# Optimization experiments

Measured on AMD Instinct MI355X. Metric: run time of the kernel, lower is better.

## Reference

```python
import jax, jax.numpy as jnp
import numpy as np
from jax import lax

B, P, NB, NF, NC, R = 128, 2048, 2000, 250, 16, 128
LS = NB - NF  # number of simulated bins = len_bins_gensig - 1


def setup_inputs() -> dict:
    key = jax.random.key(0)
    ks = jax.random.split(key, 10)
    return {
        'batched_stim_spat': jax.random.normal(ks[0], (B, P), jnp.float32),
        'stim_time': jax.random.normal(ks[1], (NB,), jnp.float32),
        'batched_initial_spike_section': (jax.random.uniform(ks[2], (B, NF)) < 0.05).astype(jnp.float32),
        'batched_coupling_cells': (jax.random.uniform(ks[3], (B, NC, NB)) < 0.05).astype(jnp.float32),
        'spatial_filter': jax.random.normal(ks[4], (P,), jnp.float32) * 0.02,
        'spatial_bias': jnp.float32(-2.0),
        'stim_timecourse_filter': jax.random.normal(ks[5], (NF,), jnp.float32) * 0.1,
        'feedback_filter': jax.random.normal(ks[6], (NF,), jnp.float32) * 0.05 - 0.02,
        'coupling_filter': jax.random.normal(ks[7], (NC, NF), jnp.float32) * 0.05,
        'u': jax.random.uniform(ks[8], (LS, B, R), jnp.float32),
        'n_repeats': R,
    }


def _corr1d_valid(x, k):
    # torch F.conv1d is cross-correlation; lax conv is too (no kernel flip)
    # x: (n,), k: (m,) -> (n - m + 1,)
    out = lax.conv_general_dilated(x[None, None, :], k[None, None, :], (1,), 'VALID',
                                   dimension_numbers=('NCH', 'OIH', 'NCH'))
    return out[0, 0]


def reference(batched_stim_spat, stim_time, batched_initial_spike_section,
              batched_coupling_cells, spatial_filter, spatial_bias,
              stim_timecourse_filter, feedback_filter, coupling_filter, u, n_repeats):
    nf = stim_timecourse_filter.shape[0]

    # stimulus time component: (n_bins - nf + 1,)
    filt_time = _corr1d_valid(stim_time, stim_timecourse_filter)

    # spatial exp arg for separable linear-spatial GLM:
    # einsum('bpt,p->bt', stim_spat[:,:,None]*filt_time, spatial_filter)
    # factors into outer product of (stim_spat @ spatial_filter) and filt_time
    stim_gensig = (batched_stim_spat @ spatial_filter)[:, None] * filt_time[None, :] + spatial_bias  # (B, T)

    # coupling exp arg: conv1d over all coupled cells -> (B, T)
    coup = lax.conv_general_dilated(batched_coupling_cells, coupling_filter[None, :, :], (1,), 'VALID',
                                    dimension_numbers=('NCH', 'OIH', 'NCH'))[:, 0, :]

    gensig_piece = stim_gensig + coup  # (B, T) with T = n_bins - nf + 1
    len_sim = gensig_piece.shape[1] - 1

    # initial feedback window: last nf spike bins, broadcast over repeats
    batch = batched_stim_spat.shape[0]
    w0 = jnp.broadcast_to(batched_initial_spike_section[:, None, :], (batch, n_repeats, nf)) + 0.0

    def step(window, xs):
        g_t, u_t = xs  # (B,), (B, R)
        fb = jnp.einsum('brk,k->br', window, feedback_filter)
        g = g_t[:, None] + fb
        spike = (u_t < jax.nn.sigmoid(g)).astype(window.dtype)  # Bernoulli(sigmoid(g))
        window = jnp.concatenate([window[:, :, 1:], spike[:, :, None]], axis=2)
        return window, spike

    xs = (jnp.swapaxes(gensig_piece[:, :len_sim], 0, 1), u[:len_sim])  # ((LS,B), (LS,B,R))
    _, spikes = lax.scan(step, w0, xs)  # spikes: (LS, B, R)

    out = jnp.concatenate([w0, jnp.moveaxis(spikes, 0, 2)], axis=2)  # (B, R, n_bins)
    return out
```

## Files before the change

### kernel.cpp

```cpp
#include <hip/hip_runtime.h>
#include <math.h>

#define B_  128
#define P_  2048
#define NB_ 2000
#define NF_ 250
#define NC_ 16
#define R_  128
#define LS_ 1750
#define NT_ 1751
#define BR_ (B_ * R_)
#define H_  16
#define NBLK_ 110

typedef int v4i __attribute__((ext_vector_type(4)));

__device__ __forceinline__ unsigned csel32(unsigned a, unsigned b, unsigned long long m) {
    unsigned r;
    asm("v_cndmask_b32 %0, %1, %2, %3" : "=v"(r) : "v"(a), "v"(b), "s"(m));
    return r;
}

__device__ __forceinline__ double dsel2(double t, unsigned long long m) {
    long long tb = __double_as_longlong(t);
    int tlo = (int)tb, thi = (int)(tb >> 32);
    int rlo, rhi;
    asm("v_cndmask_b32 %0, 0, %2, %4\n\t"
        "v_cndmask_b32 %1, 0, %3, %4"
        : "=&v"(rlo), "=&v"(rhi)
        : "v"(tlo), "v"(thi), "s"(m));
    return __longlong_as_double(((long long)(unsigned)rlo) | ((long long)rhi << 32));
}

__device__ __forceinline__ double dand(double t, int m) {
    return __longlong_as_double(__double_as_longlong(t) & (long long)m);
}

__device__ __forceinline__ double fdiv_fast(double a, double b) {
    double r;
    asm("v_rcp_f64 %0, %1" : "=v"(r) : "v"(b));
    r = fma(fma(-b, r, 1.0), r, r);
    r = fma(fma(-b, r, 1.0), r, r);
    double q = a * r;
    q = fma(fma(-b, q, a), r, q);
    return q;
}

__device__ __forceinline__ double logit_fast(float uf) {
    double u = (double)uf;
    double v = 1.0 - u;
    double qd = fdiv_fast(u, v);
    long long bits = __double_as_longlong(qd);
    int e = (int)((bits >> 52) & 0x7FF) - 1023;
    double m = __longlong_as_double((bits & 0xFFFFFFFFFFFFFLL) | 0x3FF0000000000000LL);
    if (m > 1.4142135623730951) { m *= 0.5; e += 1; }
    double s = fdiv_fast(m - 1.0, m + 1.0);
    double z = s * s;
    double Q = fma(z, fma(z, fma(z, fma(z,
        0.09090909090909091, 0.1111111111111111),
        0.14285714285714285), 0.2), 0.3333333333333333);
    double logm = fma(2.0 * s, z * Q, 2.0 * s);
    return fma((double)e, 0.6931471805599453, logm);
}

__global__ __launch_bounds__(256) void k_pre(const float* __restrict__ st,
                                             const float* __restrict__ stf,
                                             const float* __restrict__ sp,
                                             const float* __restrict__ sf,
                                             double* __restrict__ ft,
                                             double* __restrict__ sdot) {
    if (blockIdx.x < 7) {
        int t = blockIdx.x * 256 + threadIdx.x;
        if (t >= NT_) return;
        double s = 0.0;
        for (int k = 0; k < NF_; ++k) s += (double)st[t + k] * (double)stf[k];
        ft[t] = s;
    } else {
        __shared__ double red[256];
        int b = blockIdx.x - 7;
        double s = 0.0;
        for (int p = threadIdx.x; p < P_; p += 256)
            s += (double)sp[(size_t)b * P_ + p] * (double)sf[p];
        red[threadIdx.x] = s;
        __syncthreads();
        for (int off = 128; off > 0; off >>= 1) {
            if (threadIdx.x < off) red[threadIdx.x] += red[threadIdx.x + off];
            __syncthreads();
        }
        if (threadIdx.x == 0) sdot[b] = red[0];
    }
}

__global__ __launch_bounds__(256) void k_coup(const float* __restrict__ cc,
                                              const float* __restrict__ cf,
                                              const double* __restrict__ sdot,
                                              const double* __restrict__ ft,
                                              const float* __restrict__ bias,
                                              double* __restrict__ gensig) {
    __shared__ __align__(16) float  ccs[NC_ * 512];
    __shared__ __align__(16) double cfs[NC_ * 256];
    __shared__ double red[3][64][4];
    int b = blockIdx.y, t0 = blockIdx.x * 256;
    int tid = threadIdx.x, lane = tid & 63, wv = tid >> 6;

    for (int idx = tid; idx < NC_ * 128; idx += 256) {
        int c = idx >> 7, j4 = (idx & 127) * 4, src = t0 + j4;
        const float* p = cc + ((size_t)b * NC_ + c) * NB_ + src;
        float4 v;
        if (src + 3 < NB_) v = *(const float4*)p;
        else {
            v.x = (src     < NB_) ? p[0] : 0.f;
            v.y = (src + 1 < NB_) ? p[1] : 0.f;
            v.z = (src + 2 < NB_) ? p[2] : 0.f;
            v.w = (src + 3 < NB_) ? p[3] : 0.f;
        }
        *(float4*)&ccs[c * 512 + j4] = v;
    }
    for (int idx = tid; idx < NC_ * 256; idx += 256) {
        int c = idx >> 8, k = idx & 255;
        cfs[idx] = (k < NF_) ? (double)cf[c * NF_ + k] : 0.0;
    }
    __syncthreads();

    double a0 = 0, a1 = 0, a2 = 0, a3 = 0;
    int base = lane * 4;
    for (int c = wv; c < NC_; c += 4) {
        const float*  row  = &ccs[c * 512];
        const double* crow = &cfs[c * 256];
        float4 cur = *(const float4*)&row[base];
        for (int k4 = 0; k4 < 252; k4 += 4) {
            float4 nxt = *(const float4*)&row[base + k4 + 4];
            double e0 = cur.x, e1 = cur.y, e2 = cur.z, e3 = cur.w;
            double e4 = nxt.x, e5 = nxt.y, e6 = nxt.z;
            double c0 = crow[k4], c1 = crow[k4 + 1], c2 = crow[k4 + 2], c3 = crow[k4 + 3];
            a0 += e0 * c0 + e1 * c1 + e2 * c2 + e3 * c3;
            a1 += e1 * c0 + e2 * c1 + e3 * c2 + e4 * c3;
            a2 += e2 * c0 + e3 * c1 + e4 * c2 + e5 * c3;
            a3 += e3 * c0 + e4 * c1 + e5 * c2 + e6 * c3;
            cur = nxt;
        }
    }
    if (wv > 0) {
        red[wv - 1][lane][0] = a0; red[wv - 1][lane][1] = a1;
        red[wv - 1][lane][2] = a2; red[wv - 1][lane][3] = a3;
    }
    __syncthreads();
    if (wv == 0) {
        a0 += red[0][lane][0] + red[1][lane][0] + red[2][lane][0];
        a1 += red[0][lane][1] + red[1][lane][1] + red[2][lane][1];
        a2 += red[0][lane][2] + red[1][lane][2] + red[2][lane][2];
        a3 += red[0][lane][3] + red[1][lane][3] + red[2][lane][3];
        double gb = (double)bias[0];
        double sd = sdot[b];
        double accs[4] = {a0, a1, a2, a3};
        int tb = t0 + base;
        for (int i = 0; i < 4; ++i) {
            int t = tb + i;
            if (t < LS_) gensig[(size_t)b * LS_ + t] = sd * ft[t] + gb + accs[i];
        }
    }
}

__global__ __launch_bounds__(512, 2) void k_scan(const double* __restrict__ gensig,
                                                 const float* __restrict__ u,
                                                 const float* __restrict__ iss,
                                                 const float* __restrict__ ff,
                                                 float* __restrict__ out) {
    __shared__ double farT_all[4][16 * 17];
    __shared__ double luring[2][4][4 * 64];
    int tid = threadIdx.x;
    int wv = tid >> 6, l = tid & 63;
    int swv = wv & 3;
    const bool isPrep = (wv >= 4);
    int gw = blockIdx.x * 4 + swv;
    int b = gw >> 3, rbase = (gw & 7) * 16;
    double* farT = &farT_all[swv][0];

    int lw = l & 15;
    int q  = l >> 4;
    int cn = l >> 2;
    int j  = l & 3;
    int jo = 16 + j;

    const double* gs   = gensig + (size_t)b * LS_;
    const float*  up   = u + b * R_ + rbase + cn;
    float*        op   = out + ((size_t)(b * R_ + rbase + cn)) * NB_ + NF_;
    const float*  issb = iss + b * NF_;

    unsigned long long W0 = 0, W1 = 0, W2 = 0, W3 = 0;
    v4i Bf[4][6];
    double T1d = 0, T2d = 0, T3d = 0, T4d = 0, T5d = 0, T6d = 0;
    double tp7 = 0, tp8 = 0, tp9 = 0, tp10 = 0, tp11 = 0, tp12 = 0, tp13 = 0, tp14 = 0;
    double tp15 = 0;
    double thr0 = 0, thr1 = 0, thr2 = 0, thr3 = 0;
    double gprep = 0.0;
    float ur0 = 0.f, ur1 = 0.f, ur2 = 0.f, ur3 = 0.f;

    if (!isPrep) {
        for (int idx = l; idx < 16 * NF_; idx += 64) {
            int c = idx / NF_, k = idx - c * NF_;
            out[((size_t)(b * R_ + rbase + c)) * NB_ + k] = issb[k];
        }
        for (int k = 0; k < NF_; ++k) {
            unsigned long long bit = (issb[k] > 0.5f) ? 1ull : 0ull;
            if      (k <  64) W0 |= bit << k;
            else if (k < 128) W1 |= bit << (k - 64);
            else if (k < 192) W2 |= bit << (k - 128);
            else              W3 |= bit << (k - 192);
        }
        int Bword[4][6][4];
#pragma unroll
        for (int kc = 0; kc < 4; ++kc)
#pragma unroll
            for (int p = 0; p < 6; ++p)
#pragma unroll
                for (int w = 0; w < 4; ++w) Bword[kc][p][w] = 0;
#pragma unroll
        for (int kc = 0; kc < 4; ++kc) {
#pragma unroll
            for (int jj = 0; jj < 16; ++jj) {
                int k = kc * 64 + q * 16 + jj;
                int idx = k - lw;
                long long v = 0;
                if (idx >= 0 && idx < NF_)
                    v = __double2ll_rn((double)ff[idx] * 281474976710656.0);
#pragma unroll
                for (int p = 0; p < 6; ++p) {
                    int d = (int)((v + 128) & 255) - 128;
                    v = (v - (long long)d) >> 8;
                    Bword[kc][p][jj >> 2] |= (d & 255) << ((jj & 3) * 8);
                }
            }
        }
#pragma unroll
        for (int kc = 0; kc < 4; ++kc)
#pragma unroll
            for (int p = 0; p < 6; ++p) {
                v4i t; t.x = Bword[kc][p][0]; t.y = Bword[kc][p][1];
                t.z = Bword[kc][p][2]; t.w = Bword[kc][p][3];
                Bf[kc][p] = t;
            }
        T1d  = (double)ff[249]; T2d  = (double)ff[248]; T3d  = (double)ff[247];
        T4d  = (double)ff[246]; T5d  = (double)ff[245]; T6d  = (double)ff[244];
        tp7  = (double)ff[243]; tp8  = (double)ff[242]; tp9  = (double)ff[241];
        tp10 = (double)ff[240]; tp11 = (double)ff[239]; tp12 = (double)ff[238];
        tp13 = (double)ff[237]; tp14 = (double)ff[236]; tp15 = (double)ff[235];
    } else {
        ur0 = up[(size_t)(0  + j) * BR_];
        ur1 = up[(size_t)(4  + j) * BR_];
        ur2 = up[(size_t)(8  + j) * BR_];
        ur3 = up[(size_t)(12 + j) * BR_];
        luring[0][swv][  0 + l] = logit_fast(ur0);
        luring[0][swv][ 64 + l] = logit_fast(ur1);
        luring[0][swv][128 + l] = logit_fast(ur2);
        luring[0][swv][192 + l] = logit_fast(ur3);
        ur0 = up[(size_t)(16 + j) * BR_];
        ur1 = up[(size_t)(20 + j) * BR_];
        ur2 = up[(size_t)(24 + j) * BR_];
        ur3 = up[(size_t)(28 + j) * BR_];
        luring[1][swv][  0 + l] = logit_fast(ur0);
        luring[1][swv][ 64 + l] = logit_fast(ur1);
        luring[1][swv][128 + l] = logit_fast(ur2);
        luring[1][swv][192 + l] = logit_fast(ur3);
        ur0 = up[(size_t)(32 + j) * BR_];
        ur1 = up[(size_t)(36 + j) * BR_];
        ur2 = up[(size_t)(40 + j) * BR_];
        ur3 = up[(size_t)(44 + j) * BR_];
    }

    auto do_far = [&](double gp) {
        unsigned long long Sarr[4] = {W0, W1, W2, W3};
        v4i accm[6];
#pragma unroll
        for (int p = 0; p < 6; ++p) accm[p] = (v4i){0, 0, 0, 0};
#pragma unroll
        for (int kc = 0; kc < 4; ++kc) {
            unsigned f = (unsigned)((Sarr[kc] >> (q * 16)) & 0xFFFFull);
            v4i av;
            av.x = (int)((((f      ) & 0xFu) * 0x00204081u) & 0x01010101u);
            av.y = (int)((((f >>  4) & 0xFu) * 0x00204081u) & 0x01010101u);
            av.z = (int)((((f >>  8) & 0xFu) * 0x00204081u) & 0x01010101u);
            av.w = (int)((((f >> 12) & 0xFu) * 0x00204081u) & 0x01010101u);
#pragma unroll
            for (int p = 0; p < 6; ++p)
                accm[p] = __builtin_amdgcn_mfma_i32_16x16x64_i8(av, Bf[kc][p], accm[p], 0, 0, 0);
        }
#pragma unroll
        for (int r = 0; r < 4; ++r) {
            int lo = accm[0][r] + accm[1][r] * 256 + accm[2][r] * 65536;
            int hi = accm[3][r] + accm[4][r] * 256 + accm[5][r] * 65536;
            double fb = gp + (double)lo * 0x1p-48 + (double)hi * 0x1p-24;
            farT[(q * 4 + r) * 17 + lw] = fb;
        }
    };

    auto xbcalc = [&](int e4, unsigned qsnap) -> double {
        unsigned qs = qsnap >> e4;
        double x = (dand(tp7,  __builtin_amdgcn_sbfe((int)qs, jo - 7,  1)) +
                    dand(tp8,  __builtin_amdgcn_sbfe((int)qs, jo - 8,  1))) +
                   (dand(tp9,  __builtin_amdgcn_sbfe((int)qs, jo - 9,  1)) +
                    dand(tp10, __builtin_amdgcn_sbfe((int)qs, jo - 10, 1)));
        double y = (dand(tp11, __builtin_amdgcn_sbfe((int)qs, jo - 11, 1)) +
                    dand(tp12, __builtin_amdgcn_sbfe((int)qs, jo - 12, 1))) +
                   (dand(tp13, __builtin_amdgcn_sbfe((int)qs, jo - 13, 1)) +
                    dand(tp14, __builtin_amdgcn_sbfe((int)qs, jo - 14, 1)));
        return (x + y) + dand(tp15, __builtin_amdgcn_sbfe((int)qs, jo - 15, 1));
    };

    __syncthreads();

    if (!isPrep) {
        gprep = gs[lw];
        do_far(gprep);
        double lu0 = luring[0][swv][  0 + l];
        double lu1 = luring[0][swv][ 64 + l];
        double lu2 = luring[0][swv][128 + l];
        double lu3 = luring[0][swv][192 + l];
        __asm__ volatile("s_waitcnt lgkmcnt(0)" ::: "memory");
        thr0 = lu0 - farT[cn * 17 +  0 + j];
        thr1 = lu1 - farT[cn * 17 +  4 + j];
        thr2 = lu2 - farT[cn * 17 +  8 + j];
        thr3 = lu3 - farT[cn * 17 + 12 + j];
        { int tg = 16 + lw; if (tg > LS_ - 1) tg = LS_ - 1; gprep = gs[tg]; }
    }

    __syncthreads();

#define STEP(T, XB, THR) { \
    double s23 = dsel2(T2d, sp2) + dsel2(T3d, sp3); \
    double s456 = dsel2(T4d, sp4) + (dsel2(T5d, sp5) + dsel2(T6d, sp6)); \
    double X = (XB) + (s23 + s456); \
    double Y = X + T1d; \
    unsigned long long Bm0 = __ballot(X > (THR)); \
    unsigned long long Bm1 = __ballot(Y > (THR)); \
    unsigned long long b0n = (Bm0 >> ((T) & 3)) & QP; \
    unsigned long long b1n = (Bm1 >> ((T) & 3)) & QP; \
    unsigned long long sn = b0n ^ (sp1 & (b1n ^ b0n)); \
    unsigned long long fl = sn | (sn << 1); fl |= (fl << 2); \
    sp6 = sp5; sp5 = sp4; sp4 = sp3; sp3 = sp2; sp2 = sp1; sp1 = fl; \
    QL = csel32(QL, QL | (1u << (16 + (T))), fl); \
}

    int blk = 0;
    for (int t0 = 0; t0 < LS_; t0 += H_, ++blk) {
        if (!isPrep) {
            const unsigned long long QP = 0x1111111111111111ull;
            unsigned QL = 0;
            unsigned long long sp1 = 0, sp2 = 0, sp3 = 0, sp4 = 0, sp5 = 0, sp6 = 0;
            double XB0 = 0.0, XB1, XB2, XB3;
            STEP(0, XB0, thr0)
            { unsigned qs1 = QL; XB1 = xbcalc(4, qs1); }
            STEP(1, XB0, thr0)
            STEP(2, XB0, thr0)
            STEP(3, XB0, thr0)
            STEP(4, XB1, thr1)
            { unsigned qs2 = QL; XB2 = xbcalc(8, qs2); }
            STEP(5, XB1, thr1)
            STEP(6, XB1, thr1)
            STEP(7, XB1, thr1)
            STEP(8, XB2, thr2)
            { unsigned qs3 = QL; XB3 = xbcalc(12, qs3); }
            STEP(9,  XB2, thr2)
            STEP(10, XB2, thr2)
            STEP(11, XB2, thr2)
            STEP(12, XB3, thr3)
            STEP(13, XB3, thr3)
            STEP(14, XB3, thr3)
            STEP(15, XB3, thr3)
            unsigned q2 = QL >> 16;

            int rem = LS_ - t0; if (rem > H_) rem = H_;
            int s0 = 4 * j;
            if (s0 + 3 < rem) {
                float4 o;
                o.x = (float)((q2 >> (s0    )) & 1u);
                o.y = (float)((q2 >> (s0 + 1)) & 1u);
                o.z = (float)((q2 >> (s0 + 2)) & 1u);
                o.w = (float)((q2 >> (s0 + 3)) & 1u);
                *(float4*)(op + t0 + s0) = o;
            } else {
#pragma unroll
                for (int e = 0; e < 4; ++e)
                    if (s0 + e < rem) op[t0 + s0 + e] = (float)((q2 >> (s0 + e)) & 1u);
            }

            if (t0 + H_ < LS_) {
                double lu0 = luring[(blk + 1) & 1][swv][  0 + l];
                double lu1 = luring[(blk + 1) & 1][swv][ 64 + l];
                double lu2 = luring[(blk + 1) & 1][swv][128 + l];
                double lu3 = luring[(blk + 1) & 1][swv][192 + l];

                int q2i = __builtin_amdgcn_ds_bpermute(lw << 4, (int)q2);
                unsigned long long q2n = (unsigned long long)(unsigned)q2i;
                W0 = (W0 >> 16) | (W1 << 48);
                W1 = (W1 >> 16) | (W2 << 48);
                W2 = (W2 >> 16) | (W3 << 48);
                W3 = (W3 >> 16) | (q2n << 42);

                do_far(gprep);
                __asm__ volatile("s_waitcnt lgkmcnt(0)" ::: "memory");
                thr0 = lu0 - farT[cn * 17 +  0 + j];
                thr1 = lu1 - farT[cn * 17 +  4 + j];
                thr2 = lu2 - farT[cn * 17 +  8 + j];
                thr3 = lu3 - farT[cn * 17 + 12 + j];

                int tg = t0 + 32 + lw; if (tg > LS_ - 1) tg = LS_ - 1;
                gprep = gs[tg];
            }
        } else {
            if (blk <= NBLK_ - 3) {
                double lu0 = logit_fast(ur0), lu1 = logit_fast(ur1);
                double lu2 = logit_fast(ur2), lu3 = logit_fast(ur3);
                luring[blk & 1][swv][  0 + l] = lu0;
                luring[blk & 1][swv][ 64 + l] = lu1;
                luring[blk & 1][swv][128 + l] = lu2;
                luring[blk & 1][swv][192 + l] = lu3;
                if (blk <= NBLK_ - 4) {
                    int T = (blk + 3) * H_;
                    int t_;
                    t_ = T +  0 + j; if (t_ > LS_ - 1) t_ = LS_ - 1; ur0 = up[(size_t)t_ * BR_];
                    t_ = T +  4 + j; if (t_ > LS_ - 1) t_ = LS_ - 1; ur1 = up[(size_t)t_ * BR_];
                    t_ = T +  8 + j; if (t_ > LS_ - 1) t_ = LS_ - 1; ur2 = up[(size_t)t_ * BR_];
                    t_ = T + 12 + j; if (t_ > LS_ - 1) t_ = LS_ - 1; ur3 = up[(size_t)t_ * BR_];
                }
            }
        }
        __syncthreads();
    }
#undef STEP
}

extern "C" void kernel_launch(void* const* d_in, const int* in_sizes, int n_in,
                              void* d_out, int out_size, void* d_ws, size_t ws_size,
                              hipStream_t stream) {
    const float* stim_spat = (const float*)d_in[0];
    const float* stim_time = (const float*)d_in[1];
    const float* iss       = (const float*)d_in[2];
    const float* cc        = (const float*)d_in[3];
    const float* sf        = (const float*)d_in[4];
    const float* bias      = (const float*)d_in[5];
    const float* stf       = (const float*)d_in[6];
    const float* ff        = (const float*)d_in[7];
    const float* cf        = (const float*)d_in[8];
    const float* u         = (const float*)d_in[9];
    (void)in_sizes; (void)n_in; (void)out_size; (void)ws_size;

    float* out = (float*)d_out;

    double* ws     = (double*)d_ws;
    double* gensig = ws;
    double* ft     = gensig + (size_t)B_ * LS_;
    double* sdot   = ft + NT_;

    k_pre  <<<135, 256, 0, stream>>>(stim_time, stf, stim_spat, sf, ft, sdot);
    k_coup <<<dim3(7, B_), 256, 0, stream>>>(cc, cf, sdot, ft, bias, gensig);
    k_scan <<<B_ * 2, 512, 0, stream>>>(gensig, u, iss, ff, out);
}
```

Baseline: 562.7 us.

## Resolve four sequential spike steps per round via speculative ballots

Replaces the per-timestep STEP sequence, which issued two ballots per step with a serial dependency, by a ROUND that precomputes all eight speculative partial sums for the near-feedback terms of four consecutive steps. It issues eight ballots up front and then resolves the actual spikes with bitwise selects across lane columns. The aim is to shorten the serial ballot-to-ballot dependency chain inside each 16-step block. In exchange it adds more double adds, more ballots and more scalar mask logic per step group, and the correctness of the mask bookkeeping is subtle.

After: 524.6 us. 6.8% less time.

```diff
diff --git a/kernel.cpp b/kernel.cpp
--- a/kernel.cpp
+++ b/kernel.cpp
@@ -181,6 +181,12 @@
     int cn = l >> 2;
     int j  = l & 3;
     int jo = 16 + j;
+
+    const unsigned long long COL0_ = 0x1111111111111111ull;
+    const unsigned long long COL1_ = COL0_ << 1;
+    const unsigned long long COL2_ = COL0_ << 2;
+    const unsigned long long COL3_ = COL0_ << 3;
+    const unsigned long long COL01_ = COL0_ | COL1_;
 
     const double* gs   = gensig + (size_t)b * LS_;
     const float*  up   = u + b * R_ + rbase + cn;
@@ -326,47 +332,72 @@
 
     __syncthreads();
 
-#define STEP(T, XB, THR) { \
-    double s23 = dsel2(T2d, sp2) + dsel2(T3d, sp3); \
-    double s456 = dsel2(T4d, sp4) + (dsel2(T5d, sp5) + dsel2(T6d, sp6)); \
-    double X = (XB) + (s23 + s456); \
-    double Y = X + T1d; \
-    unsigned long long Bm0 = __ballot(X > (THR)); \
-    unsigned long long Bm1 = __ballot(Y > (THR)); \
-    unsigned long long b0n = (Bm0 >> ((T) & 3)) & QP; \
-    unsigned long long b1n = (Bm1 >> ((T) & 3)) & QP; \
-    unsigned long long sn = b0n ^ (sp1 & (b1n ^ b0n)); \
-    unsigned long long fl = sn | (sn << 1); fl |= (fl << 2); \
-    sp6 = sp5; sp5 = sp4; sp4 = sp3; sp3 = sp2; sp2 = sp1; sp1 = fl; \
-    QL = csel32(QL, QL | (1u << (16 + (T))), fl); \
+#define ROUND(E, XB, THR) { \
+    double d4 = dsel2(T4d, A4); \
+    double d5 = dsel2(T5d, A5); \
+    double d6 = dsel2(T6d, A6); \
+    double xb0 = (XB) + ((d4 + d5) + d6); \
+    double xb1 = xb0 + T1d; \
+    double xc0 = xb0 + T2d, xc1 = xb1 + T2d; \
+    double xd0 = xb0 + T3d, xd1 = xb1 + T3d, xd2 = xc0 + T3d, xd3 = xc1 + T3d; \
+    unsigned long long Bm0 = __ballot(xb0 > (THR)); \
+    unsigned long long Bm1 = __ballot(xb1 > (THR)); \
+    unsigned long long Bm2 = __ballot(xc0 > (THR)); \
+    unsigned long long Bm3 = __ballot(xc1 > (THR)); \
+    unsigned long long Bm4 = __ballot(xd0 > (THR)); \
+    unsigned long long Bm5 = __ballot(xd1 > (THR)); \
+    unsigned long long Bm6 = __ballot(xd2 > (THR)); \
+    unsigned long long Bm7 = __ballot(xd3 > (THR)); \
+    unsigned long long a3p = P >> 1, a2p = P >> 2; \
+    unsigned long long C0 = Bm0 ^ (a3p & (Bm4 ^ Bm0)); \
+    unsigned long long C1 = Bm1 ^ (a3p & (Bm5 ^ Bm1)); \
+    unsigned long long C2 = Bm2 ^ (a3p & (Bm6 ^ Bm2)); \
+    unsigned long long C3 = Bm3 ^ (a3p & (Bm7 ^ Bm3)); \
+    unsigned long long D0 = C0 ^ (a2p & (C2 ^ C0)); \
+    unsigned long long D1 = C1 ^ (a2p & (C3 ^ C1)); \
+    unsigned long long Dd = D1 ^ D0; \
+    unsigned long long S = (D0 ^ ((P >> 3) & Dd)) & COL0_; \
+    S |= (D0 ^ ((S << 1) & Dd)) & COL1_; \
+    { unsigned long long a2s = S << 2; \
+      unsigned long long D0b = C0 ^ (a2s & (C2 ^ C0)); \
+      unsigned long long D1b = C1 ^ (a2s & (C3 ^ C1)); \
+      S |= (D0b ^ ((S << 1) & (D1b ^ D0b))) & COL2_; } \
+    { unsigned long long a3s = S << 3, a2s = S << 2; \
+      unsigned long long C0c = Bm0 ^ (a3s & (Bm4 ^ Bm0)); \
+      unsigned long long C1c = Bm1 ^ (a3s & (Bm5 ^ Bm1)); \
+      unsigned long long C2c = Bm2 ^ (a3s & (Bm6 ^ Bm2)); \
+      unsigned long long C3c = Bm3 ^ (a3s & (Bm7 ^ Bm3)); \
+      unsigned long long D0c = C0c ^ (a2s & (C2c ^ C0c)); \
+      unsigned long long D1c = C1c ^ (a2s & (C3c ^ C1c)); \
+      S |= (D0c ^ ((S << 1) & (D1c ^ D0c))) & COL3_; } \
+    unsigned long long mm; \
+    mm = S & COL0_;        mm |= mm << 1; mm |= mm << 2; \
+    QL = csel32(QL, QL | (1u << (16 + 4 * (E) + 0)), mm); \
+    mm = (S >> 1) & COL0_; mm |= mm << 1; mm |= mm << 2; \
+    QL = csel32(QL, QL | (1u << (16 + 4 * (E) + 1)), mm); \
+    mm = (S >> 2) & COL0_; mm |= mm << 1; mm |= mm << 2; \
+    QL = csel32(QL, QL | (1u << (16 + 4 * (E) + 2)), mm); \
+    mm = (S >> 3) & COL0_; mm |= mm << 1; mm |= mm << 2; \
+    QL = csel32(QL, QL | (1u << (16 + 4 * (E) + 3)), mm); \
+    A4 = S; \
+    A5 = ((S << 1) & ~COL0_) | ((P >> 3) & COL0_); \
+    A6 = ((S << 2) & ~COL01_) | ((P >> 2) & COL01_); \
+    P = S; \
 }
 
     int blk = 0;
     for (int t0 = 0; t0 < LS_; t0 += H_, ++blk) {
         if (!isPrep) {
-            const unsigned long long QP = 0x1111111111111111ull;
             unsigned QL = 0;
-            unsigned long long sp1 = 0, sp2 = 0, sp3 = 0, sp4 = 0, sp5 = 0, sp6 = 0;
-            double XB0 = 0.0, XB1, XB2, XB3;
-            STEP(0, XB0, thr0)
-            { unsigned qs1 = QL; XB1 = xbcalc(4, qs1); }
-            STEP(1, XB0, thr0)
-            STEP(2, XB0, thr0)
-            STEP(3, XB0, thr0)
-            STEP(4, XB1, thr1)
-            { unsigned qs2 = QL; XB2 = xbcalc(8, qs2); }
-            STEP(5, XB1, thr1)
-            STEP(6, XB1, thr1)
-            STEP(7, XB1, thr1)
-            STEP(8, XB2, thr2)
-            { unsigned qs3 = QL; XB3 = xbcalc(12, qs3); }
-            STEP(9,  XB2, thr2)
-            STEP(10, XB2, thr2)
-            STEP(11, XB2, thr2)
-            STEP(12, XB3, thr3)
-            STEP(13, XB3, thr3)
-            STEP(14, XB3, thr3)
-            STEP(15, XB3, thr3)
+            unsigned long long P = 0, A4 = 0, A5 = 0, A6 = 0;
+            double XB1, XB2, XB3;
+            ROUND(0, 0.0, thr0)
+            XB1 = xbcalc(4, QL);
+            ROUND(1, XB1, thr1)
+            XB2 = xbcalc(8, QL);
+            ROUND(2, XB2, thr2)
+            XB3 = xbcalc(12, QL);
+            ROUND(3, XB3, thr3)
             unsigned q2 = QL >> 16;
 
             int rem = LS_ - t0; if (rem > H_) rem = H_;
@@ -427,7 +458,7 @@
         }
         __syncthreads();
     }
-#undef STEP
+#undef ROUND
 }
 
 extern "C" void kernel_launch(void* const* d_in, const int* in_sizes, int n_in,
```
